# Kernel tuning notes

Measured on AMD Instinct MI355X. Metric: run time of the kernel, lower is better.

## Reference

```python
import jax, jax.numpy as jnp
import numpy as np

N_NODES = 50000
N_EDGES = 800000
IN_DIM = 128
HEADS = 4
CH = 16            # hidden_dim per head
HC = HEADS * CH    # 64
N_GRAPHS = 64
NEG_SLOPE = 0.2


def gat_layer(x, edge_index, edge_attr, W, We, att_src, att_dst, att_edge, bias):
    """PyG GATConv (concat=True, edge_dim=1, eval mode: no dropout)."""
    N = x.shape[0]
    src, dst = edge_index[0], edge_index[1]
    xs = (x @ W).reshape(N, HEADS, CH)                         # [N,H,C]
    a_src = jnp.sum(xs * att_src, axis=-1)                     # [N,H]
    a_dst = jnp.sum(xs * att_dst, axis=-1)                     # [N,H]
    e = (edge_attr @ We).reshape(-1, HEADS, CH)                # [E,H,C]
    a_edge = jnp.sum(e * att_edge, axis=-1)                    # [E,H]
    alpha = a_src[src] + a_dst[dst] + a_edge                   # [E,H]
    alpha = jax.nn.leaky_relu(alpha, NEG_SLOPE)
    # segment softmax over incoming edges of each dst node
    seg_max = jax.ops.segment_max(alpha, dst, num_segments=N)  # [N,H]
    ealpha = jnp.exp(alpha - seg_max[dst])
    seg_sum = jax.ops.segment_sum(ealpha, dst, num_segments=N)
    coef = ealpha / seg_sum[dst]                               # [E,H]
    msg = xs[src] * coef[:, :, None]                           # [E,H,C]
    out = jax.ops.segment_sum(msg, dst, num_segments=N)        # [N,H,C]
    return out.reshape(N, HC) + bias


def setup_inputs() -> dict:
    key = jax.random.key(0)
    ks = jax.random.split(key, 20)
    s = 0.1
    inp = {
        "x": jax.random.normal(ks[0], (N_NODES, IN_DIM), dtype=jnp.float32),
        "edge_index": jax.random.randint(ks[1], (2, N_EDGES), 0, N_NODES, dtype=jnp.int32),
        "edge_attr": jax.random.normal(ks[2], (N_EDGES, 1), dtype=jnp.float32),
        "batch": jnp.sort(jax.random.randint(ks[3], (N_NODES,), 0, N_GRAPHS, dtype=jnp.int32)),
        # layer 1 params
        "W1": jax.random.normal(ks[4], (IN_DIM, HC), dtype=jnp.float32) * s,
        "We1": jax.random.normal(ks[5], (1, HC), dtype=jnp.float32) * s,
        "as1": jax.random.normal(ks[6], (HEADS, CH), dtype=jnp.float32) * s,
        "ad1": jax.random.normal(ks[7], (HEADS, CH), dtype=jnp.float32) * s,
        "ae1": jax.random.normal(ks[8], (HEADS, CH), dtype=jnp.float32) * s,
        "b1": jnp.zeros((HC,), dtype=jnp.float32),
        # layer 2 params (input HC)
        "W2": jax.random.normal(ks[9], (HC, HC), dtype=jnp.float32) * s,
        "We2": jax.random.normal(ks[10], (1, HC), dtype=jnp.float32) * s,
        "as2": jax.random.normal(ks[11], (HEADS, CH), dtype=jnp.float32) * s,
        "ad2": jax.random.normal(ks[12], (HEADS, CH), dtype=jnp.float32) * s,
        "ae2": jax.random.normal(ks[13], (HEADS, CH), dtype=jnp.float32) * s,
        "b2": jnp.zeros((HC,), dtype=jnp.float32),
    }
    return inp


def reference(x, edge_index, edge_attr, batch,
              W1, We1, as1, ad1, ae1, b1,
              W2, We2, as2, ad2, ae2, b2):
    h = gat_layer(x, edge_index, edge_attr, W1, We1, as1, ad1, ae1, b1)
    h = jax.nn.relu(h)                                          # dropout = identity (eval)
    h = gat_layer(h, edge_index, edge_attr, W2, We2, as2, ad2, ae2, b2)
    # global mean pool per graph
    sums = jax.ops.segment_sum(h, batch, num_segments=N_GRAPHS)           # [G,HC]
    cnt = jax.ops.segment_sum(jnp.ones((h.shape[0],), h.dtype), batch,
                              num_segments=N_GRAPHS)
    return sums / jnp.maximum(cnt, 1.0)[:, None]
```

## Files before the change

kernel.cpp:

```cpp
#include <hip/hip_runtime.h>
#include <float.h>

#define N_NODES   50000
#define N_EDGES   800000
#define INDIM1    128
#define HC        64
#define N_GRAPHS  64
#define NEG_SLOPE 0.2f
#define CAP       64
#define CSTRIDE   16

#define FGROUPS   521
#define FTBLK     (3 * FGROUPS)
#define FSBLK     (2 * FGROUPS)
#define FGRID     (5 * FGROUPS + 1)
#define ESTRIDE   (FSBLK * 256)

__global__ __launch_bounds__(256, 4) void fused1_kernel(const float* __restrict__ x,
                                                        const float* __restrict__ W,
                                                        const float* __restrict__ att_s,
                                                        const float* __restrict__ att_d,
                                                        float* __restrict__ xs,
                                                        float* __restrict__ a_src,
                                                        float* __restrict__ a_dst,
                                                        const int* __restrict__ src,
                                                        const int* __restrict__ dst,
                                                        const float* __restrict__ eattr,
                                                        int* __restrict__ cursor,
                                                        int2* __restrict__ csr_se,
                                                        const float* __restrict__ We1,
                                                        const float* __restrict__ ae1,
                                                        const float* __restrict__ We2,
                                                        const float* __restrict__ ae2,
                                                        float* __restrict__ wd) {
    constexpr int K4 = INDIM1 / 4;
    constexpr int NPW = 8;
    __shared__ float4 Wsh[K4 * 64];
    __shared__ float4 xsh[4][2][K4];
    int bid = blockIdx.x;
    int t = threadIdx.x;

    if (bid == FGRID - 1) {
        if (t < 128) {
            const float* We = (t < 64) ? We1 : We2;
            const float* ae = (t < 64) ? ae1 : ae2;
            int l = t & 63;
            float p = We[l] * ae[l];
            for (int off = 1; off < 16; off <<= 1) p += __shfl_xor(p, off);
            if ((l & 15) == 0) wd[(t >> 6) * 4 + (l >> 4)] = p;
        }
        return;
    }

    int grp = bid / 5;
    int rem = bid - grp * 5;
    if (rem >= 3) {
        int sb = grp * 2 + (rem - 3);
        for (int e = sb * 256 + t; e < N_EDGES; e += ESTRIDE) {
            int d = dst[e];
            int c = atomicAdd(&cursor[(size_t)d * CSTRIDE], 1);
            if (c < CAP)
                csr_se[(size_t)d * CAP + c] = make_int2(src[e], __float_as_int(eattr[e]));
        }
        return;
    }

    int tb = grp * 3 + rem;
    for (int i = t; i < K4 * 64; i += 256) {
        int k4 = i >> 6, col = i & 63;
        Wsh[i] = make_float4(W[(4 * k4 + 0) * 64 + col], W[(4 * k4 + 1) * 64 + col],
                             W[(4 * k4 + 2) * 64 + col], W[(4 * k4 + 3) * 64 + col]);
    }
    __syncthreads();
    int w = t >> 6, lane = t & 63;
    float avs = att_s[lane], avd = att_d[lane];
    int node0 = tb * (4 * NPW) + w * NPW;
    for (int ng = 0; ng < NPW; ng += 2) {
        int nbase = node0 + ng;
        if (nbase >= N_NODES) return;
        for (int q = lane; q < 2 * K4; q += 64) {
            int nn = q / K4, kk = q - nn * K4;
            int node = nbase + nn;
            xsh[w][nn][kk] = (node < N_NODES)
                ? ((const float4*)(x + (size_t)node * INDIM1))[kk]
                : make_float4(0.f, 0.f, 0.f, 0.f);
        }
        float acc0 = 0.f, acc1 = 0.f;
#pragma unroll 4
        for (int k4 = 0; k4 < K4; ++k4) {
            float4 wv = Wsh[k4 * 64 + lane];
            float4 x0 = xsh[w][0][k4];
            float4 x1 = xsh[w][1][k4];
            acc0 = fmaf(x0.x, wv.x, acc0);
            acc0 = fmaf(x0.y, wv.y, acc0);
            acc0 = fmaf(x0.z, wv.z, acc0);
            acc0 = fmaf(x0.w, wv.w, acc0);
            acc1 = fmaf(x1.x, wv.x, acc1);
            acc1 = fmaf(x1.y, wv.y, acc1);
            acc1 = fmaf(x1.z, wv.z, acc1);
            acc1 = fmaf(x1.w, wv.w, acc1);
        }
#pragma unroll
        for (int nn = 0; nn < 2; ++nn) {
            int node = nbase + nn;
            if (node >= N_NODES) break;
            float a = nn ? acc1 : acc0;
            xs[(size_t)node * 64 + lane] = a;
            float ps = a * avs;
            float pd = a * avd;
            for (int off = 1; off < 16; off <<= 1) {
                ps += __shfl_xor(ps, off);
                pd += __shfl_xor(pd, off);
            }
            if ((lane & 15) == 0) {
                a_src[node * 4 + (lane >> 4)] = ps;
                a_dst[node * 4 + (lane >> 4)] = pd;
            }
        }
    }
}

template <int INDIM, int NPW>
__global__ __launch_bounds__(256, 4) void transform_kernel(const float* __restrict__ x,
                                                           const float* __restrict__ W,
                                                           const float* __restrict__ att_s,
                                                           const float* __restrict__ att_d,
                                                           float* __restrict__ xs,
                                                           float* __restrict__ a_src,
                                                           float* __restrict__ a_dst) {
    constexpr int K4 = INDIM / 4;
    __shared__ float4 Wsh[K4 * 64];
    __shared__ float4 xsh[4][2][K4];
    int t = threadIdx.x;
    for (int i = t; i < K4 * 64; i += 256) {
        int k4 = i >> 6, col = i & 63;
        Wsh[i] = make_float4(W[(4 * k4 + 0) * 64 + col], W[(4 * k4 + 1) * 64 + col],
                             W[(4 * k4 + 2) * 64 + col], W[(4 * k4 + 3) * 64 + col]);
    }
    __syncthreads();
    int w = t >> 6, lane = t & 63;
    float avs = att_s[lane], avd = att_d[lane];
    int node0 = blockIdx.x * (4 * NPW) + w * NPW;
    for (int ng = 0; ng < NPW; ng += 2) {
        int nbase = node0 + ng;
        if (nbase >= N_NODES) return;
        for (int q = lane; q < 2 * K4; q += 64) {
            int nn = q / K4, kk = q - nn * K4;
            int node = nbase + nn;
            xsh[w][nn][kk] = (node < N_NODES)
                ? ((const float4*)(x + (size_t)node * INDIM))[kk]
                : make_float4(0.f, 0.f, 0.f, 0.f);
        }
        float acc0 = 0.f, acc1 = 0.f;
#pragma unroll 4
        for (int k4 = 0; k4 < K4; ++k4) {
            float4 wv = Wsh[k4 * 64 + lane];
            float4 x0 = xsh[w][0][k4];
            float4 x1 = xsh[w][1][k4];
            acc0 = fmaf(x0.x, wv.x, acc0);
            acc0 = fmaf(x0.y, wv.y, acc0);
            acc0 = fmaf(x0.z, wv.z, acc0);
            acc0 = fmaf(x0.w, wv.w, acc0);
            acc1 = fmaf(x1.x, wv.x, acc1);
            acc1 = fmaf(x1.y, wv.y, acc1);
            acc1 = fmaf(x1.z, wv.z, acc1);
            acc1 = fmaf(x1.w, wv.w, acc1);
        }
#pragma unroll
        for (int nn = 0; nn < 2; ++nn) {
            int node = nbase + nn;
            if (node >= N_NODES) break;
            float a = nn ? acc1 : acc0;
            xs[(size_t)node * 64 + lane] = a;
            float ps = a * avs;
            float pd = a * avd;
            for (int off = 1; off < 16; off <<= 1) {
                ps += __shfl_xor(ps, off);
                pd += __shfl_xor(pd, off);
            }
            if ((lane & 15) == 0) {
                a_src[node * 4 + (lane >> 4)] = ps;
                a_dst[node * 4 + (lane >> 4)] = pd;
            }
        }
    }
}

__global__ __launch_bounds__(256) void aggregate_kernel(const float* __restrict__ xs,
                                                        const int2* __restrict__ csr_se,
                                                        const int* __restrict__ degp,
                                                        const float* __restrict__ a_src,
                                                        const float* __restrict__ a_dst,
                                                        const float* __restrict__ wd,
                                                        const float* __restrict__ bias,
                                                        float* __restrict__ outb,
                                                        int do_relu) {
    int w = threadIdx.x >> 6, lane = threadIdx.x & 63;
    int node = blockIdx.x * 4 + w;
    if (node >= N_NODES) return;
    int beg = node * CAP;
    int end = beg + min(degp[(size_t)node * CSTRIDE], CAP);
    const int e_idx = lane >> 2;
    const int h4 = lane & 3;
    const int h2 = lane >> 4;

    float wdv = wd[h4];
    float adv = a_dst[node * 4 + h4];

    float m = -FLT_MAX;
    float s = 0.f;
    float acc = 0.f;

    for (int j0 = beg; j0 < end; j0 += 16) {
        int j = j0 + e_idx;
        bool v = (j < end);
        int sv = 0;
        float a = -FLT_MAX;
        if (v) {
            int2 se = csr_se[j];
            sv = se.x;
            float ea = __int_as_float(se.y);
            float as = a_src[sv * 4 + h4];
            a = as + adv + ea * wdv;
            a = a > 0.f ? a : NEG_SLOPE * a;
        }
        float cm = a;
        cm = fmaxf(cm, __shfl_xor(cm, 4));
        cm = fmaxf(cm, __shfl_xor(cm, 8));
        cm = fmaxf(cm, __shfl_xor(cm, 16));
        cm = fmaxf(cm, __shfl_xor(cm, 32));
        float mn = fmaxf(m, cm);
        float sc = __expf(m - mn);
        float wgt = __expf(a - mn);
        s = s * sc + wgt;
        m = mn;
        acc *= __shfl(sc, h2);
#pragma unroll
        for (int e = 0; e < 16; ++e) {
            float wg = __shfl(wgt, (e << 2) | h2);
            int svb = __shfl(sv, e << 2);
            acc = fmaf(wg, xs[(size_t)svb * 64 + lane], acc);
        }
    }
    s += __shfl_xor(s, 4);
    s += __shfl_xor(s, 8);
    s += __shfl_xor(s, 16);
    s += __shfl_xor(s, 32);
    float sh = __shfl(s, h2);
    float res = (sh > 0.f) ? acc / sh : 0.f;
    res += bias[lane];
    if (do_relu) res = fmaxf(res, 0.f);
    outb[(size_t)node * 64 + lane] = res;
}

__global__ __launch_bounds__(256) void pool_kernel(const float* __restrict__ h,
                                                   const int* __restrict__ batch,
                                                   float* __restrict__ out) {
    int wave = (blockIdx.x * blockDim.x + threadIdx.x) >> 6;
    int lane = threadIdx.x & 63;
    int i0 = wave * 16;
    if (i0 >= N_NODES) return;
    int i1 = min(i0 + 16, N_NODES);
    float acc = 0.f;
    int gcur = batch[i0];
    for (int i = i0; i < i1; ++i) {
        int g = batch[i];
        if (g != gcur) {
            atomicAdd(&out[gcur * 64 + lane], acc);
            acc = 0.f; gcur = g;
        }
        acc += h[i * 64 + lane];
    }
    atomicAdd(&out[gcur * 64 + lane], acc);
}

__global__ void pool_div_kernel(float* __restrict__ out, const int* __restrict__ batch) {
    int g = blockIdx.x, t = threadIdx.x;
    int lo = 0, hi = N_NODES;
    while (lo < hi) { int mid = (lo + hi) >> 1; if (batch[mid] < g) lo = mid + 1; else hi = mid; }
    int lo2 = lo, hi2 = N_NODES;
    while (lo2 < hi2) { int mid = (lo2 + hi2) >> 1; if (batch[mid] <= g) lo2 = mid + 1; else hi2 = mid; }
    float c = (float)max(lo2 - lo, 1);
    out[g * 64 + t] /= c;
}


extern "C" void kernel_launch(void* const* d_in, const int* in_sizes, int n_in,
                              void* d_out, int out_size, void* d_ws, size_t ws_size,
                              hipStream_t stream) {
    const float* x    = (const float*)d_in[0];
    const int*   eidx = (const int*)d_in[1];
    const float* eat  = (const float*)d_in[2];
    const int*   batch= (const int*)d_in[3];
    const float* W1   = (const float*)d_in[4];
    const float* We1  = (const float*)d_in[5];
    const float* as1  = (const float*)d_in[6];
    const float* ad1  = (const float*)d_in[7];
    const float* ae1  = (const float*)d_in[8];
    const float* b1   = (const float*)d_in[9];
    const float* W2   = (const float*)d_in[10];
    const float* We2  = (const float*)d_in[11];
    const float* as2  = (const float*)d_in[12];
    const float* ad2  = (const float*)d_in[13];
    const float* ae2  = (const float*)d_in[14];
    const float* b2   = (const float*)d_in[15];
    const int* src  = eidx;
    const int* dstp = eidx + N_EDGES;
    float* out = (float*)d_out;

    char* p = (char*)d_ws;
    auto alloc = [&](size_t bytes) {
        char* r = p;
        p += (bytes + 255) & ~(size_t)255;
        return r;
    };
    int2*  csrse  = (int2*)alloc((size_t)N_NODES * CAP * 8);
    float* xs     = (float*)alloc((size_t)N_NODES * 64 * 4);
    float* hbuf   = (float*)alloc((size_t)N_NODES * 64 * 4);
    float* asrc   = (float*)alloc((size_t)N_NODES * 4 * 4);
    float* adst   = (float*)alloc((size_t)N_NODES * 4 * 4);
    float* wd     = (float*)alloc(64);
    int*   cursor = (int*)alloc((size_t)N_NODES * CSTRIDE * 4);

    hipMemsetAsync(cursor, 0, (size_t)N_NODES * CSTRIDE * 4, stream);
    hipMemsetAsync(d_out, 0, (size_t)N_GRAPHS * 64 * 4, stream);

    const int NPW = 8;
    const int TB = (N_NODES + 4 * NPW - 1) / (4 * NPW);
    const int NB = (N_NODES + 3) / 4;

    fused1_kernel<<<FGRID, 256, 0, stream>>>(x, W1, as1, ad1, xs, asrc, adst,
                                             src, dstp, eat, cursor, csrse,
                                             We1, ae1, We2, ae2, wd);
    aggregate_kernel<<<NB, 256, 0, stream>>>(xs, csrse, cursor, asrc, adst,
                                             wd, b1, hbuf, 1);
    transform_kernel<HC, NPW><<<TB, 256, 0, stream>>>(hbuf, W2, as2, ad2, xs, asrc, adst);
    aggregate_kernel<<<NB, 256, 0, stream>>>(xs, csrse, cursor, asrc, adst,
                                             wd + 4, b2, hbuf, 0);
    int pool_waves = (N_NODES + 15) / 16;
    int pool_blocks = (pool_waves + 3) / 4;
    pool_kernel<<<pool_blocks, 256, 0, stream>>>(hbuf, batch, out);
    pool_div_kernel<<<N_GRAPHS, 64, 0, stream>>>(out, batch);
}
```

Baseline: 269.5 us.

## Process two nodes per wave in aggregation and fuse mean-pool into second layer

Each wave in the aggregate kernel now handles two destination nodes, interleaving their alpha and gather phases so that more independent gathers are in flight. The second-layer aggregation accumulates its outputs straight into the per-graph pool using block-level LDS reduction and atomics. This removes the separate pool kernel and the hbuf write and read for layer 2. Source-index broadcast now uses readlane instead of shfl, and the launch bound asks for 6 blocks per CU. NB = N_NODES/8 relies on N_NODES being divisible by 8, and the __syncthreads sits inside a branch that is uniform per block.

```diff
diff --git a/kernel.cpp b/kernel.cpp
--- a/kernel.cpp
+++ b/kernel.cpp
@@ -186,35 +186,44 @@
     }
 }
 
-__global__ __launch_bounds__(256) void aggregate_kernel(const float* __restrict__ xs,
-                                                        const int2* __restrict__ csr_se,
-                                                        const int* __restrict__ degp,
-                                                        const float* __restrict__ a_src,
-                                                        const float* __restrict__ a_dst,
-                                                        const float* __restrict__ wd,
-                                                        const float* __restrict__ bias,
-                                                        float* __restrict__ outb,
-                                                        int do_relu) {
-    int w = threadIdx.x >> 6, lane = threadIdx.x & 63;
-    int node = blockIdx.x * 4 + w;
-    if (node >= N_NODES) return;
-    int beg = node * CAP;
-    int end = beg + min(degp[(size_t)node * CSTRIDE], CAP);
+template <int POOL>
+__global__ __launch_bounds__(256, 6) void aggregate_kernel(const float* __restrict__ xs,
+                                                           const int2* __restrict__ csr_se,
+                                                           const int* __restrict__ degp,
+                                                           const float* __restrict__ a_src,
+                                                           const float* __restrict__ a_dst,
+                                                           const float* __restrict__ wd,
+                                                           const float* __restrict__ bias,
+                                                           float* __restrict__ outb,
+                                                           int do_relu,
+                                                           const int* __restrict__ batch,
+                                                           float* __restrict__ gout) {
+    __shared__ float plds[256];
+    int t = threadIdx.x;
+    int w = t >> 6, lane = t & 63;
     const int e_idx = lane >> 2;
     const int h4 = lane & 3;
     const int h2 = lane >> 4;
+    int nodeA = blockIdx.x * 8 + w * 2;
+    int nodeB = nodeA + 1;
 
     float wdv = wd[h4];
-    float adv = a_dst[node * 4 + h4];
-
-    float m = -FLT_MAX;
-    float s = 0.f;
-    float acc = 0.f;
-
-    for (int j0 = beg; j0 < end; j0 += 16) {
-        int j = j0 + e_idx;
-        bool v = (j < end);
-        int sv = 0;
+    float bv = bias[lane];
+    float advA = a_dst[nodeA * 4 + h4];
+    float advB = a_dst[nodeB * 4 + h4];
+    int nA = min(degp[(size_t)nodeA * CSTRIDE], CAP);
+    int nB = min(degp[(size_t)nodeB * CSTRIDE], CAP);
+    int begA = nodeA * CAP, endA = begA + nA;
+    int begB = nodeB * CAP, endB = begB + nB;
+
+    float mA = -FLT_MAX, sA = 0.f, accA = 0.f;
+    float mB = -FLT_MAX, sB = 0.f, accB = 0.f;
+
+    auto alpha_phase = [&](int beg, int end, int it, float adv,
+                           float& m, float& s, float& acc, int& sv, float& wgt) {
+        int j = beg + it * 16 + e_idx;
+        bool v = j < end;
+        sv = 0;
         float a = -FLT_MAX;
         if (v) {
             int2 se = csr_se[j];
@@ -231,47 +240,77 @@
         cm = fmaxf(cm, __shfl_xor(cm, 32));
         float mn = fmaxf(m, cm);
         float sc = __expf(m - mn);
-        float wgt = __expf(a - mn);
+        wgt = __expf(a - mn);
         s = s * sc + wgt;
         m = mn;
         acc *= __shfl(sc, h2);
+    };
+    auto gather_phase = [&](int sv, float wgt, float& acc) {
 #pragma unroll
         for (int e = 0; e < 16; ++e) {
+            int svb = __builtin_amdgcn_readlane(sv, e << 2);
             float wg = __shfl(wgt, (e << 2) | h2);
-            int svb = __shfl(sv, e << 2);
             acc = fmaf(wg, xs[(size_t)svb * 64 + lane], acc);
         }
-    }
-    s += __shfl_xor(s, 4);
-    s += __shfl_xor(s, 8);
-    s += __shfl_xor(s, 16);
-    s += __shfl_xor(s, 32);
-    float sh = __shfl(s, h2);
-    float res = (sh > 0.f) ? acc / sh : 0.f;
-    res += bias[lane];
-    if (do_relu) res = fmaxf(res, 0.f);
-    outb[(size_t)node * 64 + lane] = res;
-}
-
-__global__ __launch_bounds__(256) void pool_kernel(const float* __restrict__ h,
-                                                   const int* __restrict__ batch,
-                                                   float* __restrict__ out) {
-    int wave = (blockIdx.x * blockDim.x + threadIdx.x) >> 6;
-    int lane = threadIdx.x & 63;
-    int i0 = wave * 16;
-    if (i0 >= N_NODES) return;
-    int i1 = min(i0 + 16, N_NODES);
-    float acc = 0.f;
-    int gcur = batch[i0];
-    for (int i = i0; i < i1; ++i) {
-        int g = batch[i];
-        if (g != gcur) {
-            atomicAdd(&out[gcur * 64 + lane], acc);
-            acc = 0.f; gcur = g;
-        }
-        acc += h[i * 64 + lane];
-    }
-    atomicAdd(&out[gcur * 64 + lane], acc);
+    };
+
+    int itA = (nA + 15) >> 4, itB = (nB + 15) >> 4;
+    int itC = min(itA, itB);
+    for (int it = 0; it < itC; ++it) {
+        int svA, svB; float wgtA, wgtB;
+        alpha_phase(begA, endA, it, advA, mA, sA, accA, svA, wgtA);
+        alpha_phase(begB, endB, it, advB, mB, sB, accB, svB, wgtB);
+        gather_phase(svA, wgtA, accA);
+        gather_phase(svB, wgtB, accB);
+    }
+    for (int it = itC; it < itA; ++it) {
+        int svA; float wgtA;
+        alpha_phase(begA, endA, it, advA, mA, sA, accA, svA, wgtA);
+        gather_phase(svA, wgtA, accA);
+    }
+    for (int it = itC; it < itB; ++it) {
+        int svB; float wgtB;
+        alpha_phase(begB, endB, it, advB, mB, sB, accB, svB, wgtB);
+        gather_phase(svB, wgtB, accB);
+    }
+
+    auto finish = [&](float s, float acc) {
+        s += __shfl_xor(s, 4);
+        s += __shfl_xor(s, 8);
+        s += __shfl_xor(s, 16);
+        s += __shfl_xor(s, 32);
+        float sh = __shfl(s, h2);
+        float res = (sh > 0.f) ? acc / sh : 0.f;
+        return res + bv;
+    };
+    float resA = finish(sA, accA);
+    float resB = finish(sB, accB);
+
+    if (POOL) {
+        int gA = batch[nodeA], gB = batch[nodeB];
+        int gF = batch[blockIdx.x * 8];
+        int gL = batch[blockIdx.x * 8 + 7];
+        if (gF == gL) {
+            plds[w * 64 + lane] = resA + resB;
+            __syncthreads();
+            if (w == 0) {
+                float v = plds[lane] + plds[64 + lane] +
+                          plds[128 + lane] + plds[192 + lane];
+                atomicAdd(&gout[gF * 64 + lane], v);
+            }
+        } else {
+            if (gA == gB) {
+                atomicAdd(&gout[gA * 64 + lane], resA + resB);
+            } else {
+                atomicAdd(&gout[gA * 64 + lane], resA);
+                atomicAdd(&gout[gB * 64 + lane], resB);
+            }
+        }
+    } else {
+        if (do_relu) { resA = fmaxf(resA, 0.f); resB = fmaxf(resB, 0.f); }
+        outb[(size_t)nodeA * 64 + lane] = resA;
+        outb[(size_t)nodeB * 64 + lane] = resB;
+    }
 }
 
 __global__ void pool_div_kernel(float* __restrict__ out, const int* __restrict__ batch) {
@@ -327,18 +366,15 @@
 
     const int NPW = 8;
     const int TB = (N_NODES + 4 * NPW - 1) / (4 * NPW);
-    const int NB = (N_NODES + 3) / 4;
+    const int NB = N_NODES / 8;
 
     fused1_kernel<<<FGRID, 256, 0, stream>>>(x, W1, as1, ad1, xs, asrc, adst,
                                              src, dstp, eat, cursor, csrse,
                                              We1, ae1, We2, ae2, wd);
-    aggregate_kernel<<<NB, 256, 0, stream>>>(xs, csrse, cursor, asrc, adst,
-                                             wd, b1, hbuf, 1);
+    aggregate_kernel<0><<<NB, 256, 0, stream>>>(xs, csrse, cursor, asrc, adst,
+                                                wd, b1, hbuf, 1, nullptr, nullptr);
     transform_kernel<HC, NPW><<<TB, 256, 0, stream>>>(hbuf, W2, as2, ad2, xs, asrc, adst);
-    aggregate_kernel<<<NB, 256, 0, stream>>>(xs, csrse, cursor, asrc, adst,
-                                             wd + 4, b2, hbuf, 0);
-    int pool_waves = (N_NODES + 15) / 16;
-    int pool_blocks = (pool_waves + 3) / 4;
-    pool_kernel<<<pool_blocks, 256, 0, stream>>>(hbuf, batch, out);
+    aggregate_kernel<1><<<NB, 256, 0, stream>>>(xs, csrse, cursor, asrc, adst,
+                                                wd + 4, b2, nullptr, 0, batch, out);
     pool_div_kernel<<<N_GRAPHS, 64, 0, stream>>>(out, batch);
 }
```

Result: faster. 250.5 us (-7.1%).
